# Performance work log

Measured on AMD Instinct MI355X. Metric: run time of the kernel, lower is better.

Reference implementation:

```python
import jax, jax.numpy as jnp
import numpy as np

N_NODES = 100_000
N_EDGES = 1_600_000
IN_DIM = 512
HID = 128
OUT_DIM = 40


def setup_inputs() -> dict:
    key = jax.random.key(0)
    ks = jax.random.split(key, 12)
    s = 0.05  # small init scale
    x = jax.random.normal(ks[0], (N_NODES, IN_DIM), dtype=jnp.float32)
    edge_index = jax.random.randint(ks[1], (2, N_EDGES), 0, N_NODES, dtype=jnp.int64)
    W1 = jax.random.normal(ks[2], (IN_DIM, HID), dtype=jnp.float32) * s
    b1 = jnp.zeros((HID,), jnp.float32)
    Wg0 = jax.random.normal(ks[3], (HID, HID), dtype=jnp.float32) * s
    bg0 = jnp.zeros((HID,), jnp.float32)
    Wg1 = jax.random.normal(ks[4], (HID, HID), dtype=jnp.float32) * s
    bg1 = jnp.zeros((HID,), jnp.float32)
    W2 = jax.random.normal(ks[5], (HID, OUT_DIM), dtype=jnp.float32) * s
    b2 = jnp.zeros((OUT_DIM,), jnp.float32)
    return dict(x=x, edge_index=edge_index, W1=W1, b1=b1, Wg0=Wg0, bg0=bg0,
                Wg1=Wg1, bg1=bg1, W2=W2, b2=b2)


def _gcn_norm(edge_index, num_nodes, dtype):
    # PyG GCNConv default: add self-loops, symmetric normalization D^-1/2 A D^-1/2.
    loops = jnp.arange(num_nodes, dtype=edge_index.dtype)
    src = jnp.concatenate([edge_index[0], loops])  # [E+N]
    dst = jnp.concatenate([edge_index[1], loops])
    deg = jax.ops.segment_sum(jnp.ones(dst.shape, dtype), dst, num_segments=num_nodes)
    dinv = jnp.where(deg > 0, jax.lax.rsqrt(deg), jnp.zeros((), dtype))
    norm = dinv[src] * dinv[dst]  # [E+N]
    return src, dst, norm


def _gcn_conv(h, src, dst, norm, W, b, num_nodes):
    # out[dst] += norm * (h @ W)[src]; then bias
    hw = h @ W                              # [N, HID]
    msg = hw[src] * norm[:, None]           # gather + scale  [E+N, HID]
    agg = jax.ops.segment_sum(msg, dst, num_segments=num_nodes)  # scatter-add
    return agg + b


def reference(x, edge_index, W1, b1, Wg0, bg0, Wg1, bg1, W2, b2):
    n = x.shape[0]
    src, dst, norm = _gcn_norm(edge_index, n, x.dtype)
    h = jax.nn.relu(x @ W1 + b1)  # dropout is identity in eval mode
    for W, b in ((Wg0, bg0), (Wg1, bg1)):
        h = jax.nn.relu(_gcn_conv(h, src, dst, norm, W, b, n))
    logits = h @ W2 + b2
    return jax.nn.log_softmax(logits, axis=1)
```

## Files before the change

kernel.cpp:

```cpp
#include <hip/hip_runtime.h>
#include <hip/hip_bf16.h>
#include <cstdint>

#define HID 128

typedef short s16x8 __attribute__((ext_vector_type(8)));
typedef float f32x4 __attribute__((ext_vector_type(4)));

static inline size_t align_up(size_t x, size_t a) { return (x + a - 1) & ~(a - 1); }

__device__ inline ushort f2bf(float f) {
  uint u = __float_as_uint(f);
  u += 0x7FFFu + ((u >> 16) & 1u);
  return (ushort)(u >> 16);
}
__device__ inline uint pk2bf(float lo, float hi) {
  __hip_bfloat162 h = __float22bfloat162_rn(float2{lo, hi});
  return *reinterpret_cast<uint*>(&h);
}
__device__ inline float bf2f_lo(uint v) { return __uint_as_float(v << 16); }
__device__ inline float bf2f_hi(uint v) { return __uint_as_float(v & 0xFFFF0000u); }

__global__ void detect_i64_kernel(const unsigned int* __restrict__ p, int nwords,
                                  int* __restrict__ flag) {
  __shared__ int any;
  if (threadIdx.x == 0) any = 0;
  __syncthreads();
  for (int i = threadIdx.x; i < 1024; i += blockDim.x) {
    int w = 2 * i + 1;
    if (w < nwords && p[w] != 0u) atomicOr(&any, 1);
  }
  __syncthreads();
  if (threadIdx.x == 0) *flag = (any == 0) ? 1 : 0;
}

__global__ void extract_count_kernel(const void* __restrict__ ei, const int* __restrict__ flag,
                                     int E, int* __restrict__ src32, int* __restrict__ dst32,
                                     int* __restrict__ cnt) {
  int e = blockIdx.x * blockDim.x + threadIdx.x;
  if (e >= E) return;
  int s, d;
  if (*flag) {
    const long long* p = (const long long*)ei;
    s = (int)p[e];
    d = (int)p[(size_t)E + e];
  } else {
    const int* p = (const int*)ei;
    s = p[e];
    d = p[(size_t)E + e];
  }
  src32[e] = s;
  dst32[e] = d;
  atomicAdd(&cnt[d], 1);
}

__global__ void dinv_kernel(const int* __restrict__ cnt, float* __restrict__ dinv, int N) {
  int i = blockIdx.x * blockDim.x + threadIdx.x;
  if (i >= N) return;
  dinv[i] = rsqrtf((float)(cnt[i] + 1));
}

__global__ __launch_bounds__(1024) void scan_local_kernel(const int* __restrict__ cnt,
    int* __restrict__ off, int* __restrict__ bsum, int N) {
  __shared__ int buf[1024];
  int tid = threadIdx.x;
  int i = blockIdx.x * 1024 + tid;
  int v = (i < N) ? cnt[i] : 0;
  buf[tid] = v;
  __syncthreads();
  #pragma unroll
  for (int s = 1; s < 1024; s <<= 1) {
    int t = (tid >= s) ? buf[tid - s] : 0;
    __syncthreads();
    buf[tid] += t;
    __syncthreads();
  }
  if (i < N) off[i] = buf[tid] - v;
  if (tid == 1023) bsum[blockIdx.x] = buf[1023];
}

__global__ __launch_bounds__(128) void scan_bsum_kernel(const int* __restrict__ bsum, int nb,
    int* __restrict__ boff, int* __restrict__ offN) {
  __shared__ int b[128];
  int tid = threadIdx.x;
  int v = (tid < nb) ? bsum[tid] : 0;
  b[tid] = v;
  __syncthreads();
  #pragma unroll
  for (int s = 1; s < 128; s <<= 1) {
    int t = (tid >= s) ? b[tid - s] : 0;
    __syncthreads();
    b[tid] += t;
    __syncthreads();
  }
  if (tid < nb) boff[tid] = b[tid] - v;
  if (tid == 127) *offN = b[127];
}

__global__ void scan_add_kernel(int* __restrict__ off, const int* __restrict__ boff,
                                int* __restrict__ cursor, int N) {
  int i = blockIdx.x * blockDim.x + threadIdx.x;
  if (i >= N) return;
  int o = off[i] + boff[i >> 10];
  off[i] = o;
  cursor[i] = o;
}

__global__ void fill_kernel(const int* __restrict__ src32, const int* __restrict__ dst32,
                            const float* __restrict__ dinv, int* __restrict__ cursor,
                            int* __restrict__ csr_src, float* __restrict__ csr_norm, int E) {
  int e = blockIdx.x * blockDim.x + threadIdx.x;
  if (e >= E) return;
  int s = src32[e];
  int d = dst32[e];
  int pos = atomicAdd(&cursor[d], 1);
  csr_src[pos] = s;
  csr_norm[pos] = dinv[s] * dinv[d];
}

__global__ void convert_w_kernel(const float* __restrict__ W, ushort* __restrict__ Wt,
                                 int K, int KP) {
  int id = blockIdx.x * blockDim.x + threadIdx.x;
  if (id >= K * 128) return;
  int c = id & 127;
  int k = id >> 7;
  Wt[(size_t)c * KP + k] = f2bf(W[id]);
}

__global__ void convert_w2_kernel(const float* __restrict__ W2, ushort* __restrict__ Wt) {
  int id = blockIdx.x * blockDim.x + threadIdx.x;
  if (id >= 48 * 128) return;
  int c = id >> 7;
  int k = id & 127;
  Wt[(size_t)c * 128 + k] = (c < 40) ? f2bf(W2[(size_t)k * 40 + c]) : (ushort)0;
}

template <int K, bool AF32, bool BIAS_RELU, int WAVES>
__global__ __launch_bounds__(WAVES * 64, (WAVES == 16) ? 4 : 16 / WAVES)
void gemm_lds_kernel(
    const void* __restrict__ Ap, const ushort* __restrict__ Wtp,
    const float* __restrict__ bias, ushort* __restrict__ outp,
    int M, int rowsPerBlock) {
  constexpr int KP = K + 8;
  extern __shared__ __align__(16) ushort lB[];
  const int tid = threadIdx.x;

  const int rowStart = blockIdx.x * rowsPerBlock;
  if (rowStart >= M) return;
  const int rowEnd = min(M, rowStart + rowsPerBlock);

  constexpr int TOTC = 128 * KP / 8;
  const s16x8* Wt8 = (const s16x8*)Wtp;
  for (int i = tid; i < TOTC; i += WAVES * 64) ((s16x8*)lB)[i] = Wt8[i];
  __syncthreads();

  const int w = tid >> 6;
  const int l = tid & 63;
  const int l15 = l & 15;
  const int kg = l >> 4;

  const ushort* Ab = (const ushort*)Ap;
  const float* Af = (const float*)Ap;

  for (int base = rowStart + w * 16; base < rowEnd; base += WAVES * 16) {
    int row = base + l15;
    if (row >= M) row = M - 1;

    f32x4 acc[8];
    #pragma unroll
    for (int c = 0; c < 8; ++c) acc[c] = f32x4{0.f, 0.f, 0.f, 0.f};

    #pragma unroll 4
    for (int k0 = 0; k0 < K; k0 += 32) {
      s16x8 af;
      if constexpr (AF32) {
        const float* s = &Af[(size_t)row * K + k0 + kg * 8];
        float4 v0 = *(const float4*)s;
        float4 v1 = *(const float4*)(s + 4);
        uint4 u;
        u.x = pk2bf(v0.x, v0.y);
        u.y = pk2bf(v0.z, v0.w);
        u.z = pk2bf(v1.x, v1.y);
        u.w = pk2bf(v1.z, v1.w);
        af = *reinterpret_cast<s16x8*>(&u);
      } else {
        af = *(const s16x8*)&Ab[(size_t)row * K + k0 + kg * 8];
      }
      #pragma unroll
      for (int c = 0; c < 8; ++c) {
        s16x8 bfr = *(const s16x8*)&lB[(16 * c + l15) * KP + k0 + kg * 8];
        acc[c] = __builtin_amdgcn_mfma_f32_16x16x32_bf16(af, bfr, acc[c], 0, 0, 0);
      }
    }

    #pragma unroll
    for (int c = 0; c < 8; ++c) {
      float b = 0.f;
      if constexpr (BIAS_RELU) b = bias[16 * c + l15];
      #pragma unroll
      for (int v = 0; v < 4; ++v) {
        int r = base + kg * 4 + v;
        if (r < M) {
          float val = acc[c][v];
          if constexpr (BIAS_RELU) val = fmaxf(val + b, 0.f);
          outp[(size_t)r * 128 + 16 * c + l15] = f2bf(val);
        }
      }
    }
  }
}

__global__ __launch_bounds__(256) void aggregate_bf16_kernel(const ushort* __restrict__ hw,
    const int* __restrict__ off, const int* __restrict__ csr_src,
    const float* __restrict__ csr_norm, const float* __restrict__ dinv,
    const float* __restrict__ bias, ushort* __restrict__ out, int N) {
  int wid = (blockIdx.x * blockDim.x + threadIdx.x) >> 6;
  int lane = threadIdx.x & 63;
  if (wid >= N) return;
  const uint* hw4 = (const uint*)hw;
  int beg = off[wid], end = off[wid + 1];
  float ax = 0.f, ay = 0.f;
  int j = beg;
  for (; j + 4 <= end; j += 4) {
    int s0 = csr_src[j];
    int s1 = csr_src[j + 1];
    int s2 = csr_src[j + 2];
    int s3 = csr_src[j + 3];
    float n0 = csr_norm[j];
    float n1 = csr_norm[j + 1];
    float n2 = csr_norm[j + 2];
    float n3 = csr_norm[j + 3];
    uint v0 = hw4[(size_t)s0 * 64 + lane];
    uint v1 = hw4[(size_t)s1 * 64 + lane];
    uint v2 = hw4[(size_t)s2 * 64 + lane];
    uint v3 = hw4[(size_t)s3 * 64 + lane];
    ax = fmaf(n0, bf2f_lo(v0), ax); ay = fmaf(n0, bf2f_hi(v0), ay);
    ax = fmaf(n1, bf2f_lo(v1), ax); ay = fmaf(n1, bf2f_hi(v1), ay);
    ax = fmaf(n2, bf2f_lo(v2), ax); ay = fmaf(n2, bf2f_hi(v2), ay);
    ax = fmaf(n3, bf2f_lo(v3), ax); ay = fmaf(n3, bf2f_hi(v3), ay);
  }
  for (; j < end; ++j) {
    int s = csr_src[j];
    float nm = csr_norm[j];
    uint v = hw4[(size_t)s * 64 + lane];
    ax = fmaf(nm, bf2f_lo(v), ax);
    ay = fmaf(nm, bf2f_hi(v), ay);
  }
  float di = dinv[wid];
  float snm = di * di;
  uint v = hw4[(size_t)wid * 64 + lane];
  ax = fmaf(snm, bf2f_lo(v), ax);
  ay = fmaf(snm, bf2f_hi(v), ay);
  float2 b = ((const float2*)bias)[lane];
  float ox = fmaxf(ax + b.x, 0.f);
  float oy = fmaxf(ay + b.y, 0.f);
  ((uint*)out)[(size_t)wid * 64 + lane] = pk2bf(ox, oy);
}

__global__ __launch_bounds__(256) void final_mfma_kernel(const ushort* __restrict__ h,
    const ushort* __restrict__ W2t, const float* __restrict__ b2,
    float* __restrict__ out, int M) {
  const int tid = threadIdx.x;
  const int w = tid >> 6;
  const int l = tid & 63;
  const int l15 = l & 15;
  const int kg = l >> 4;
  const int base = (blockIdx.x * 4 + w) * 16;
  if (base >= M) return;
  int row = base + l15;
  if (row >= M) row = M - 1;

  f32x4 acc[3];
  #pragma unroll
  for (int c = 0; c < 3; ++c) acc[c] = f32x4{0.f, 0.f, 0.f, 0.f};

  #pragma unroll
  for (int k0 = 0; k0 < 128; k0 += 32) {
    s16x8 af = *(const s16x8*)&h[(size_t)row * 128 + k0 + kg * 8];
    #pragma unroll
    for (int c = 0; c < 3; ++c) {
      s16x8 bfr = *(const s16x8*)&W2t[(size_t)(16 * c + l15) * 128 + k0 + kg * 8];
      acc[c] = __builtin_amdgcn_mfma_f32_16x16x32_bf16(af, bfr, acc[c], 0, 0, 0);
    }
  }

  float bv0 = b2[l15];
  float bv1 = b2[16 + l15];
  float bv2 = (l15 < 8) ? b2[32 + l15] : 0.f;

  #pragma unroll
  for (int v = 0; v < 4; ++v) {
    float l0 = acc[0][v] + bv0;
    float l1 = acc[1][v] + bv1;
    float l2 = (l15 < 8) ? (acc[2][v] + bv2) : -1e30f;
    float pm = fmaxf(fmaxf(l0, l1), l2);
    #pragma unroll
    for (int sh = 8; sh > 0; sh >>= 1) pm = fmaxf(pm, __shfl_xor(pm, sh));
    float es = expf(l0 - pm) + expf(l1 - pm) + ((l15 < 8) ? expf(l2 - pm) : 0.f);
    #pragma unroll
    for (int sh = 8; sh > 0; sh >>= 1) es += __shfl_xor(es, sh);
    float lse = pm + logf(es);
    int r = base + kg * 4 + v;
    if (r < M) {
      out[(size_t)r * 40 + l15] = l0 - lse;
      out[(size_t)r * 40 + 16 + l15] = l1 - lse;
      if (l15 < 8) out[(size_t)r * 40 + 32 + l15] = l2 - lse;
    }
  }
}

extern "C" void kernel_launch(void* const* d_in, const int* in_sizes, int n_in,
                              void* d_out, int out_size, void* d_ws, size_t ws_size,
                              hipStream_t stream) {
  const float* x   = (const float*)d_in[0];
  const void*  ei  = d_in[1];
  const float* W1  = (const float*)d_in[2];
  const float* b1  = (const float*)d_in[3];
  const float* Wg0 = (const float*)d_in[4];
  const float* bg0 = (const float*)d_in[5];
  const float* Wg1 = (const float*)d_in[6];
  const float* bg1 = (const float*)d_in[7];
  const float* W2  = (const float*)d_in[8];
  const float* b2  = (const float*)d_in[9];
  float* out = (float*)d_out;

  const int N = in_sizes[0] / 512;
  const int E = in_sizes[1] / 2;

  char* wsb = (char*)d_ws;
  size_t o = 0;
  auto alloc = [&](size_t bytes) -> void* {
    void* p = wsb + o;
    o = align_up(o + bytes, 256);
    return p;
  };
  int*    flag    = (int*)alloc(4);
  int*    src32   = (int*)alloc((size_t)E * 4);
  int*    dst32   = (int*)alloc((size_t)E * 4);
  int*    cnt     = (int*)alloc((size_t)N * 4);
  float*  dinv    = (float*)alloc((size_t)N * 4);
  int*    off     = (int*)alloc((size_t)(N + 1) * 4);
  int*    cursor  = (int*)alloc((size_t)N * 4);
  int*    bsum    = (int*)alloc(128 * 4);
  int*    boff    = (int*)alloc(128 * 4);
  int*    csr_src = (int*)alloc((size_t)E * 4);
  float*  csr_nrm = (float*)alloc((size_t)E * 4);
  ushort* W1t     = (ushort*)alloc((size_t)128 * 520 * 2);
  ushort* Wg0t    = (ushort*)alloc((size_t)128 * 136 * 2);
  ushort* Wg1t    = (ushort*)alloc((size_t)128 * 136 * 2);
  ushort* W2t     = (ushort*)alloc((size_t)48 * 128 * 2);
  ushort* hb1     = (ushort*)alloc((size_t)N * HID * 2);
  ushort* hb2     = (ushort*)alloc((size_t)N * HID * 2);
  (void)ws_size; (void)n_in; (void)out_size;

  const int tpb = 256;
  const int ebl = (E + tpb - 1) / tpb;
  const int nbl = (N + tpb - 1) / tpb;

  detect_i64_kernel<<<1, 256, 0, stream>>>((const unsigned int*)ei, 2 * E, flag);
  hipMemsetAsync(cnt, 0, (size_t)N * 4, stream);
  extract_count_kernel<<<ebl, tpb, 0, stream>>>(ei, flag, E, src32, dst32, cnt);
  dinv_kernel<<<nbl, tpb, 0, stream>>>(cnt, dinv, N);
  const int nsb = (N + 1023) / 1024;
  scan_local_kernel<<<nsb, 1024, 0, stream>>>(cnt, off, bsum, N);
  scan_bsum_kernel<<<1, 128, 0, stream>>>(bsum, nsb, boff, off + N);
  scan_add_kernel<<<nbl, tpb, 0, stream>>>(off, boff, cursor, N);
  fill_kernel<<<ebl, tpb, 0, stream>>>(src32, dst32, dinv, cursor, csr_src, csr_nrm, E);

  convert_w_kernel<<<(512 * 128 + 255) / 256, 256, 0, stream>>>(W1, W1t, 512, 520);
  convert_w_kernel<<<(128 * 128 + 255) / 256, 256, 0, stream>>>(Wg0, Wg0t, 128, 136);
  convert_w_kernel<<<(128 * 128 + 255) / 256, 256, 0, stream>>>(Wg1, Wg1t, 128, 136);
  convert_w2_kernel<<<(48 * 128 + 255) / 256, 256, 0, stream>>>(W2, W2t);

  const size_t lds512 = (size_t)128 * 520 * 2;
  const size_t lds128 = (size_t)128 * 136 * 2;
  static bool attr_done = false;
  if (!attr_done) {
    (void)hipFuncSetAttribute(
        reinterpret_cast<const void*>(&gemm_lds_kernel<512, true, true, 16>),
        hipFuncAttributeMaxDynamicSharedMemorySize, (int)lds512);
    attr_done = true;
  }

  int rpb512 = (N + 255) / 256;
  rpb512 = (rpb512 + 15) & ~15;
  const int grid512 = (N + rpb512 - 1) / rpb512;
  const int rpb128 = 128;
  const int grid128 = (N + rpb128 - 1) / rpb128;
  const int abl = (N * 64 + tpb - 1) / tpb;
  const int fbl = (N + 63) / 64;

  gemm_lds_kernel<512, true, true, 16><<<grid512, 1024, lds512, stream>>>(
      x, W1t, b1, hb1, N, rpb512);

  gemm_lds_kernel<128, false, false, 4><<<grid128, 256, lds128, stream>>>(
      hb1, Wg0t, nullptr, hb2, N, rpb128);
  aggregate_bf16_kernel<<<abl, tpb, 0, stream>>>(hb2, off, csr_src, csr_nrm, dinv, bg0, hb1, N);

  gemm_lds_kernel<128, false, false, 4><<<grid128, 256, lds128, stream>>>(
      hb1, Wg1t, nullptr, hb2, N, rpb128);
  aggregate_bf16_kernel<<<abl, tpb, 0, stream>>>(hb2, off, csr_src, csr_nrm, dinv, bg1, hb1, N);

  final_mfma_kernel<<<fbl, 256, 0, stream>>>(hb1, W2t, b2, out, N);
}
```

Baseline: 481.9 us.

## Interleave CSR src/norm, unroll aggregation by 8, prefetch GEMM A operands

Packs the edge source/destination pair and the CSR source/norm pair into int2 arrays, so each edge is one 8-byte load instead of two separate loads. The aggregation loop is unrolled to 8 neighbours to keep more independent gathers in flight. The fp32 GEMM software-prefetches the next A chunk, and the bf16 GEMM loads the whole A row into registers before the MFMA loop. The costs are higher register pressure and some extra tail-handling code.

```diff
diff --git a/kernel.cpp b/kernel.cpp
--- a/kernel.cpp
+++ b/kernel.cpp
@@ -35,8 +35,7 @@
 }
 
 __global__ void extract_count_kernel(const void* __restrict__ ei, const int* __restrict__ flag,
-                                     int E, int* __restrict__ src32, int* __restrict__ dst32,
-                                     int* __restrict__ cnt) {
+                                     int E, int2* __restrict__ sd, int* __restrict__ cnt) {
   int e = blockIdx.x * blockDim.x + threadIdx.x;
   if (e >= E) return;
   int s, d;
@@ -49,8 +48,7 @@
     s = p[e];
     d = p[(size_t)E + e];
   }
-  src32[e] = s;
-  dst32[e] = d;
+  sd[e] = int2{s, d};
   atomicAdd(&cnt[d], 1);
 }
 
@@ -106,16 +104,14 @@
   cursor[i] = o;
 }
 
-__global__ void fill_kernel(const int* __restrict__ src32, const int* __restrict__ dst32,
-                            const float* __restrict__ dinv, int* __restrict__ cursor,
-                            int* __restrict__ csr_src, float* __restrict__ csr_norm, int E) {
+__global__ void fill_kernel(const int2* __restrict__ sd, const float* __restrict__ dinv,
+                            int* __restrict__ cursor, int2* __restrict__ csr, int E) {
   int e = blockIdx.x * blockDim.x + threadIdx.x;
   if (e >= E) return;
-  int s = src32[e];
-  int d = dst32[e];
-  int pos = atomicAdd(&cursor[d], 1);
-  csr_src[pos] = s;
-  csr_norm[pos] = dinv[s] * dinv[d];
+  int2 p = sd[e];
+  int pos = atomicAdd(&cursor[p.y], 1);
+  float nm = dinv[p.x] * dinv[p.y];
+  csr[pos] = int2{p.x, __float_as_int(nm)};
 }
 
 __global__ void convert_w_kernel(const float* __restrict__ W, ushort* __restrict__ Wt,
@@ -170,26 +166,41 @@
     #pragma unroll
     for (int c = 0; c < 8; ++c) acc[c] = f32x4{0.f, 0.f, 0.f, 0.f};
 
-    #pragma unroll 4
-    for (int k0 = 0; k0 < K; k0 += 32) {
-      s16x8 af;
-      if constexpr (AF32) {
-        const float* s = &Af[(size_t)row * K + k0 + kg * 8];
-        float4 v0 = *(const float4*)s;
-        float4 v1 = *(const float4*)(s + 4);
+    if constexpr (AF32) {
+      const float* ar = &Af[(size_t)row * K + kg * 8];
+      float4 p0 = *(const float4*)ar;
+      float4 p1 = *(const float4*)(ar + 4);
+      #pragma unroll 4
+      for (int k0 = 0; k0 < K; k0 += 32) {
+        float4 c0 = p0, c1 = p1;
+        if (k0 + 32 < K) {
+          p0 = *(const float4*)(ar + k0 + 32);
+          p1 = *(const float4*)(ar + k0 + 36);
+        }
         uint4 u;
-        u.x = pk2bf(v0.x, v0.y);
-        u.y = pk2bf(v0.z, v0.w);
-        u.z = pk2bf(v1.x, v1.y);
-        u.w = pk2bf(v1.z, v1.w);
-        af = *reinterpret_cast<s16x8*>(&u);
-      } else {
-        af = *(const s16x8*)&Ab[(size_t)row * K + k0 + kg * 8];
+        u.x = pk2bf(c0.x, c0.y);
+        u.y = pk2bf(c0.z, c0.w);
+        u.z = pk2bf(c1.x, c1.y);
+        u.w = pk2bf(c1.z, c1.w);
+        s16x8 af = *reinterpret_cast<s16x8*>(&u);
+        #pragma unroll
+        for (int c = 0; c < 8; ++c) {
+          s16x8 bfr = *(const s16x8*)&lB[(16 * c + l15) * KP + k0 + kg * 8];
+          acc[c] = __builtin_amdgcn_mfma_f32_16x16x32_bf16(af, bfr, acc[c], 0, 0, 0);
+        }
       }
+    } else {
+      s16x8 afs[K / 32];
       #pragma unroll
-      for (int c = 0; c < 8; ++c) {
-        s16x8 bfr = *(const s16x8*)&lB[(16 * c + l15) * KP + k0 + kg * 8];
-        acc[c] = __builtin_amdgcn_mfma_f32_16x16x32_bf16(af, bfr, acc[c], 0, 0, 0);
+      for (int k0 = 0; k0 < K; k0 += 32)
+        afs[k0 / 32] = *(const s16x8*)&Ab[(size_t)row * K + k0 + kg * 8];
+      #pragma unroll
+      for (int k0 = 0; k0 < K; k0 += 32) {
+        #pragma unroll
+        for (int c = 0; c < 8; ++c) {
+          s16x8 bfr = *(const s16x8*)&lB[(16 * c + l15) * KP + k0 + kg * 8];
+          acc[c] = __builtin_amdgcn_mfma_f32_16x16x32_bf16(afs[k0 / 32], bfr, acc[c], 0, 0, 0);
+        }
       }
     }
 
@@ -211,9 +222,9 @@
 }
 
 __global__ __launch_bounds__(256) void aggregate_bf16_kernel(const ushort* __restrict__ hw,
-    const int* __restrict__ off, const int* __restrict__ csr_src,
-    const float* __restrict__ csr_norm, const float* __restrict__ dinv,
-    const float* __restrict__ bias, ushort* __restrict__ out, int N) {
+    const int* __restrict__ off, const int2* __restrict__ csr,
+    const float* __restrict__ dinv, const float* __restrict__ bias,
+    ushort* __restrict__ out, int N) {
   int wid = (blockIdx.x * blockDim.x + threadIdx.x) >> 6;
   int lane = threadIdx.x & 63;
   if (wid >= N) return;
@@ -221,28 +232,52 @@
   int beg = off[wid], end = off[wid + 1];
   float ax = 0.f, ay = 0.f;
   int j = beg;
-  for (; j + 4 <= end; j += 4) {
-    int s0 = csr_src[j];
-    int s1 = csr_src[j + 1];
-    int s2 = csr_src[j + 2];
-    int s3 = csr_src[j + 3];
-    float n0 = csr_norm[j];
-    float n1 = csr_norm[j + 1];
-    float n2 = csr_norm[j + 2];
-    float n3 = csr_norm[j + 3];
-    uint v0 = hw4[(size_t)s0 * 64 + lane];
-    uint v1 = hw4[(size_t)s1 * 64 + lane];
-    uint v2 = hw4[(size_t)s2 * 64 + lane];
-    uint v3 = hw4[(size_t)s3 * 64 + lane];
+  int n8 = beg + ((end - beg) & ~7);
+  for (; j < n8; j += 8) {
+    int2 c0 = csr[j];     int2 c1 = csr[j + 1];
+    int2 c2 = csr[j + 2]; int2 c3 = csr[j + 3];
+    int2 c4 = csr[j + 4]; int2 c5 = csr[j + 5];
+    int2 c6 = csr[j + 6]; int2 c7 = csr[j + 7];
+    uint v0 = hw4[(size_t)c0.x * 64 + lane];
+    uint v1 = hw4[(size_t)c1.x * 64 + lane];
+    uint v2 = hw4[(size_t)c2.x * 64 + lane];
+    uint v3 = hw4[(size_t)c3.x * 64 + lane];
+    uint v4 = hw4[(size_t)c4.x * 64 + lane];
+    uint v5 = hw4[(size_t)c5.x * 64 + lane];
+    uint v6 = hw4[(size_t)c6.x * 64 + lane];
+    uint v7 = hw4[(size_t)c7.x * 64 + lane];
+    float n0 = __int_as_float(c0.y), n1 = __int_as_float(c1.y);
+    float n2 = __int_as_float(c2.y), n3 = __int_as_float(c3.y);
+    float n4 = __int_as_float(c4.y), n5 = __int_as_float(c5.y);
+    float n6 = __int_as_float(c6.y), n7 = __int_as_float(c7.y);
     ax = fmaf(n0, bf2f_lo(v0), ax); ay = fmaf(n0, bf2f_hi(v0), ay);
     ax = fmaf(n1, bf2f_lo(v1), ax); ay = fmaf(n1, bf2f_hi(v1), ay);
     ax = fmaf(n2, bf2f_lo(v2), ax); ay = fmaf(n2, bf2f_hi(v2), ay);
     ax = fmaf(n3, bf2f_lo(v3), ax); ay = fmaf(n3, bf2f_hi(v3), ay);
+    ax = fmaf(n4, bf2f_lo(v4), ax); ay = fmaf(n4, bf2f_hi(v4), ay);
+    ax = fmaf(n5, bf2f_lo(v5), ax); ay = fmaf(n5, bf2f_hi(v5), ay);
+    ax = fmaf(n6, bf2f_lo(v6), ax); ay = fmaf(n6, bf2f_hi(v6), ay);
+    ax = fmaf(n7, bf2f_lo(v7), ax); ay = fmaf(n7, bf2f_hi(v7), ay);
+  }
+  if (j + 4 <= end) {
+    int2 c0 = csr[j];     int2 c1 = csr[j + 1];
+    int2 c2 = csr[j + 2]; int2 c3 = csr[j + 3];
+    uint v0 = hw4[(size_t)c0.x * 64 + lane];
+    uint v1 = hw4[(size_t)c1.x * 64 + lane];
+    uint v2 = hw4[(size_t)c2.x * 64 + lane];
+    uint v3 = hw4[(size_t)c3.x * 64 + lane];
+    float n0 = __int_as_float(c0.y), n1 = __int_as_float(c1.y);
+    float n2 = __int_as_float(c2.y), n3 = __int_as_float(c3.y);
+    ax = fmaf(n0, bf2f_lo(v0), ax); ay = fmaf(n0, bf2f_hi(v0), ay);
+    ax = fmaf(n1, bf2f_lo(v1), ax); ay = fmaf(n1, bf2f_hi(v1), ay);
+    ax = fmaf(n2, bf2f_lo(v2), ax); ay = fmaf(n2, bf2f_hi(v2), ay);
+    ax = fmaf(n3, bf2f_lo(v3), ax); ay = fmaf(n3, bf2f_hi(v3), ay);
+    j += 4;
   }
   for (; j < end; ++j) {
-    int s = csr_src[j];
-    float nm = csr_norm[j];
-    uint v = hw4[(size_t)s * 64 + lane];
+    int2 c = csr[j];
+    float nm = __int_as_float(c.y);
+    uint v = hw4[(size_t)c.x * 64 + lane];
     ax = fmaf(nm, bf2f_lo(v), ax);
     ay = fmaf(nm, bf2f_hi(v), ay);
   }
@@ -335,16 +370,14 @@
     return p;
   };
   int*    flag    = (int*)alloc(4);
-  int*    src32   = (int*)alloc((size_t)E * 4);
-  int*    dst32   = (int*)alloc((size_t)E * 4);
+  int2*   sd      = (int2*)alloc((size_t)E * 8);
   int*    cnt     = (int*)alloc((size_t)N * 4);
   float*  dinv    = (float*)alloc((size_t)N * 4);
   int*    off     = (int*)alloc((size_t)(N + 1) * 4);
   int*    cursor  = (int*)alloc((size_t)N * 4);
   int*    bsum    = (int*)alloc(128 * 4);
   int*    boff    = (int*)alloc(128 * 4);
-  int*    csr_src = (int*)alloc((size_t)E * 4);
-  float*  csr_nrm = (float*)alloc((size_t)E * 4);
+  int2*   csr     = (int2*)alloc((size_t)E * 8);
   ushort* W1t     = (ushort*)alloc((size_t)128 * 520 * 2);
   ushort* Wg0t    = (ushort*)alloc((size_t)128 * 136 * 2);
   ushort* Wg1t    = (ushort*)alloc((size_t)128 * 136 * 2);
@@ -359,13 +392,13 @@
 
   detect_i64_kernel<<<1, 256, 0, stream>>>((const unsigned int*)ei, 2 * E, flag);
   hipMemsetAsync(cnt, 0, (size_t)N * 4, stream);
-  extract_count_kernel<<<ebl, tpb, 0, stream>>>(ei, flag, E, src32, dst32, cnt);
+  extract_count_kernel<<<ebl, tpb, 0, stream>>>(ei, flag, E, sd, cnt);
   dinv_kernel<<<nbl, tpb, 0, stream>>>(cnt, dinv, N);
   const int nsb = (N + 1023) / 1024;
   scan_local_kernel<<<nsb, 1024, 0, stream>>>(cnt, off, bsum, N);
   scan_bsum_kernel<<<1, 128, 0, stream>>>(bsum, nsb, boff, off + N);
   scan_add_kernel<<<nbl, tpb, 0, stream>>>(off, boff, cursor, N);
-  fill_kernel<<<ebl, tpb, 0, stream>>>(src32, dst32, dinv, cursor, csr_src, csr_nrm, E);
+  fill_kernel<<<ebl, tpb, 0, stream>>>(sd, dinv, cursor, csr, E);
 
   convert_w_kernel<<<(512 * 128 + 255) / 256, 256, 0, stream>>>(W1, W1t, 512, 520);
   convert_w_kernel<<<(128 * 128 + 255) / 256, 256, 0, stream>>>(Wg0, Wg0t, 128, 136);
@@ -395,11 +428,11 @@
 
   gemm_lds_kernel<128, false, false, 4><<<grid128, 256, lds128, stream>>>(
       hb1, Wg0t, nullptr, hb2, N, rpb128);
-  aggregate_bf16_kernel<<<abl, tpb, 0, stream>>>(hb2, off, csr_src, csr_nrm, dinv, bg0, hb1, N);
+  aggregate_bf16_kernel<<<abl, tpb, 0, stream>>>(hb2, off, csr, dinv, bg0, hb1, N);
 
   gemm_lds_kernel<128, false, false, 4><<<grid128, 256, lds128, stream>>>(
       hb1, Wg1t, nullptr, hb2, N, rpb128);
-  aggregate_bf16_kernel<<<abl, tpb, 0, stream>>>(hb2, off, csr_src, csr_nrm, dinv, bg1, hb1, N);
+  aggregate_bf16_kernel<<<abl, tpb, 0, stream>>>(hb2, off, csr, dinv, bg1, hb1, N);
 
   final_mfma_kernel<<<fbl, 256, 0, stream>>>(hb1, W2t, b2, out, N);
 }
```

Measured after the change: 474.1 us. No clear change (-1.6%).
